# Optimization experiments

Measured on AMD Instinct MI355X. Metric: run time of the kernel, lower is better.

Reference implementation:

```python
import jax, jax.numpy as jnp
import numpy as np

B, T, D, H = 2, 2048, 768, 12
HS = D // H           # head_size = 64
FF = 4 * D            # feed_forward_multiplier = 4 -> hidden 3072
HALF = FF // 2        # SwiGLU halves hidden -> 1536
EPS = 1e-8


def rmsnorm(x, scale):
    # RMSNorm with p=-1: full-dim L2 norm / sqrt(d), then x/(rms+eps)*scale
    d = x.shape[-1]
    rms = jnp.linalg.norm(x, axis=-1, keepdims=True) * (d ** -0.5)
    return scale * (x / (rms + EPS))


def setup_inputs() -> dict:
    key = jax.random.key(0)
    ks = jax.random.split(key, 12)
    s = 0.02
    return {
        "x":  jax.random.normal(ks[0], (B, T, D), dtype=jnp.float32),
        "Wq": jax.random.normal(ks[1], (H, D, HS), dtype=jnp.float32) * s,
        "Wk": jax.random.normal(ks[2], (H, D, HS), dtype=jnp.float32) * s,
        "Wv": jax.random.normal(ks[3], (H, D, HS), dtype=jnp.float32) * s,
        "Wo": jax.random.normal(ks[4], (D, D), dtype=jnp.float32) * s,
        "bo": jnp.zeros((D,), dtype=jnp.float32),
        "W1": jax.random.normal(ks[5], (D, FF), dtype=jnp.float32) * s,
        "b1": jnp.zeros((FF,), dtype=jnp.float32),
        "W2": jax.random.normal(ks[6], (HALF, D), dtype=jnp.float32) * s,
        "b2": jnp.zeros((D,), dtype=jnp.float32),
        "g1": jnp.ones((D,), dtype=jnp.float32),
        "g2": jnp.ones((D,), dtype=jnp.float32),
    }


def reference(x, Wq, Wk, Wv, Wo, bo, W1, b1, W2, b2, g1, g2):
    Bx, Tx, Dx = x.shape
    # --- Multi-head causal attention (pre-RMSNorm, residual) ---
    h = rmsnorm(x, g1)
    q = jnp.einsum('btd,hdk->bhtk', h, Wq)
    k = jnp.einsum('btd,hdk->bhtk', h, Wk)
    v = jnp.einsum('btd,hdk->bhtk', h, Wv)
    # NOTE: original scales by C**-0.5 where C = embed_dim (not head_size)
    scores = jnp.einsum('bhtk,bhsk->bhts', q, k) * (Dx ** -0.5)
    causal = jnp.tril(jnp.ones((Tx, Tx), dtype=bool))
    scores = jnp.where(causal, scores, -jnp.inf)
    wei = jax.nn.softmax(scores, axis=-1)
    attn = jnp.einsum('bhts,bhsk->bhtk', wei, v)
    attn = attn.transpose(0, 2, 1, 3).reshape(Bx, Tx, Dx)  # concat heads
    x = x + attn @ Wo + bo
    # --- SwiGLU FFN (pre-RMSNorm, residual) ---
    h2 = rmsnorm(x, g2)
    u = h2 @ W1 + b1
    a, gate = jnp.split(u, 2, axis=-1)  # chunk: first half = value, second = gate
    x = x + (jax.nn.silu(gate) * a) @ W2 + b2
    return x
```

## Files before the change

kernel.cpp:

```cpp
#include <hip/hip_runtime.h>
#include <math.h>

#define TDIM 2048
#define DDIM 768
#define NH   12
#define NROWS 4096
#define EPSV 1e-8f
#define SCALE 0.03608439182435161f

typedef __bf16 bf16_t;
typedef bf16_t bf16x8 __attribute__((ext_vector_type(8)));
typedef bf16_t bf16x4 __attribute__((ext_vector_type(4)));
typedef float  floatx4 __attribute__((ext_vector_type(4)));

__device__ __forceinline__ void glds16(const bf16_t* g, bf16_t* l) {
    __builtin_amdgcn_global_load_lds(
        (const __attribute__((address_space(1))) void*)g,
        (__attribute__((address_space(3))) void*)l, 16, 0, 0);
}

__global__ __launch_bounds__(256) void pack_all(
    const float* __restrict__ Wq, const float* __restrict__ Wk,
    const float* __restrict__ Wv, const float* __restrict__ Wo,
    const float* __restrict__ W1, const float* __restrict__ W2,
    bf16_t* __restrict__ qkvw, bf16_t* __restrict__ wo,
    bf16_t* __restrict__ w1, bf16_t* __restrict__ w2)
{
    int bid = blockIdx.x;
    const float* src; bf16_t* dst;
    int srcld, dstld, k0, n0;
    if (bid < 144) {
        int kx = bid % 12, nx = bid / 12;
        src = Wo; dst = wo; srcld = 768; dstld = 768; k0 = kx * 64; n0 = nx * 64;
    } else if (bid < 720) {
        int t = bid - 144; int kx = t % 12, nx = t / 12;
        src = W1; dst = w1; srcld = 3072; dstld = 768; k0 = kx * 64; n0 = nx * 64;
    } else if (bid < 1008) {
        int t = bid - 720; int kx = t % 24, nx = t / 24;
        src = W2; dst = w2; srcld = 768; dstld = 1536; k0 = kx * 64; n0 = nx * 64;
    } else {
        int t = bid - 1008; int kx = t % 12, y = t / 12;
        int sel = y / 12, h = y - sel * 12;
        src = ((sel == 0) ? Wq : (sel == 1) ? Wk : Wv) + (size_t)h * 768 * 64;
        dst = qkvw + (size_t)(sel * 768 + h * 64) * 768;
        srcld = 64; dstld = 768; k0 = kx * 64; n0 = 0;
    }
    __shared__ float Ts[64][65];
    int tid = threadIdx.x;
    int r = tid >> 2, c = (tid & 3) * 16;
    const float* s = src + (size_t)(k0 + r) * srcld + n0 + c;
    #pragma unroll
    for (int i = 0; i < 4; i++) {
        float4 t = *(const float4*)(s + i * 4);
        Ts[r][c + i*4 + 0] = t.x; Ts[r][c + i*4 + 1] = t.y;
        Ts[r][c + i*4 + 2] = t.z; Ts[r][c + i*4 + 3] = t.w;
    }
    __syncthreads();
    int n = tid >> 2, kk = (tid & 3) * 16;
    bf16x8 o0, o1;
    #pragma unroll
    for (int i = 0; i < 8; i++) {
        o0[i] = (bf16_t)Ts[kk + i][n];
        o1[i] = (bf16_t)Ts[kk + 8 + i][n];
    }
    bf16_t* d = dst + (size_t)(n0 + n) * dstld + k0 + kk;
    *(bf16x8*)d = o0;
    *(bf16x8*)(d + 8) = o1;
}

__global__ __launch_bounds__(256) void rmsnorm_bf(
    const float* __restrict__ x, const float* __restrict__ g,
    bf16_t* __restrict__ out)
{
    int row = blockIdx.x;
    int tid = threadIdx.x;
    const float* xr = x + (size_t)row * DDIM;
    float v0 = xr[tid], v1 = xr[tid + 256], v2 = xr[tid + 512];
    float s = v0*v0 + v1*v1 + v2*v2;
    #pragma unroll
    for (int off = 32; off > 0; off >>= 1)
        s += __shfl_down(s, off, 64);
    __shared__ float red[4];
    __shared__ float tot;
    if ((tid & 63) == 0) red[tid >> 6] = s;
    __syncthreads();
    if (tid == 0) tot = red[0] + red[1] + red[2] + red[3];
    __syncthreads();
    float rms = sqrtf(tot * (1.0f / DDIM));
    float inv = 1.0f / (rms + EPSV);
    bf16_t* orow = out + (size_t)row * DDIM;
    orow[tid]       = (bf16_t)(g[tid]       * v0 * inv);
    orow[tid + 256] = (bf16_t)(g[tid + 256] * v1 * inv);
    orow[tid + 512] = (bf16_t)(g[tid + 512] * v2 * inv);
}

template<int TM>
__global__ __launch_bounds__(256) void gemm_bf16(
    const bf16_t* __restrict__ A, const bf16_t* __restrict__ BT, int K,
    float* __restrict__ Cf, bf16_t* __restrict__ Cb, int ldc,
    const float* __restrict__ bias, const float* __restrict__ resid)
{
    constexpr int MT = TM / 32;
    __shared__ bf16_t As0[TM][32], As1[TM][32];
    __shared__ bf16_t Bs0[128][32], Bs1[128][32];
    int tid = threadIdx.x;
    int wave = tid >> 6, lane = tid & 63;
    int lrow = lane & 15, quad = lane >> 4;
    int wm = wave >> 1, wn = wave & 1;

    int m0 = blockIdx.y * TM;
    int n0 = blockIdx.x * 128;

    int srow = lane >> 2, scol = (lane & 3) * 8;
    const bf16_t* Ag = A  + ((size_t)m0 + wave * (TM/4) + srow) * K + scol;
    const bf16_t* Bg = BT + ((size_t)n0 + wave * 32 + srow) * K + scol;

    floatx4 acc[MT][4];
    #pragma unroll
    for (int mt = 0; mt < MT; mt++)
        #pragma unroll
        for (int nt = 0; nt < 4; nt++)
            #pragma unroll
            for (int r = 0; r < 4; r++) acc[mt][nt][r] = 0.f;

    for (int k0 = 0; k0 < K; k0 += 64) {
        __syncthreads();
        #pragma unroll
        for (int i = 0; i < TM/64; i++) {
            glds16(Ag + (size_t)(i*16) * K + k0,      &As0[wave*(TM/4) + i*16][0]);
            glds16(Ag + (size_t)(i*16) * K + k0 + 32, &As1[wave*(TM/4) + i*16][0]);
        }
        #pragma unroll
        for (int i = 0; i < 2; i++) {
            glds16(Bg + (size_t)(i*16) * K + k0,      &Bs0[wave*32 + i*16][0]);
            glds16(Bg + (size_t)(i*16) * K + k0 + 32, &Bs1[wave*32 + i*16][0]);
        }
        __syncthreads();

        bf16x8 af0[MT], af1[MT], bf0[4], bf1[4];
        #pragma unroll
        for (int mt = 0; mt < MT; mt++) {
            af0[mt] = *(const bf16x8*)&As0[wm*(TM/2) + mt*16 + lrow][quad * 8];
            af1[mt] = *(const bf16x8*)&As1[wm*(TM/2) + mt*16 + lrow][quad * 8];
        }
        #pragma unroll
        for (int nt = 0; nt < 4; nt++) {
            bf0[nt] = *(const bf16x8*)&Bs0[wn*64 + nt*16 + lrow][quad * 8];
            bf1[nt] = *(const bf16x8*)&Bs1[wn*64 + nt*16 + lrow][quad * 8];
        }
        #pragma unroll
        for (int mt = 0; mt < MT; mt++)
            #pragma unroll
            for (int nt = 0; nt < 4; nt++) {
                acc[mt][nt] = __builtin_amdgcn_mfma_f32_16x16x32_bf16(
                    bf0[nt], af0[mt], acc[mt][nt], 0, 0, 0);
                acc[mt][nt] = __builtin_amdgcn_mfma_f32_16x16x32_bf16(
                    bf1[nt], af1[mt], acc[mt][nt], 0, 0, 0);
            }
    }

    int crow0 = m0 + wm * (TM/2);
    int ccol0 = n0 + wn * 64;
    #pragma unroll
    for (int mt = 0; mt < MT; mt++) {
        int row = crow0 + mt * 16 + lrow;
        #pragma unroll
        for (int nt = 0; nt < 4; nt++) {
            int col = ccol0 + nt * 16 + quad * 4;
            size_t off = (size_t)row * ldc + col;
            float4 bv = make_float4(0.f, 0.f, 0.f, 0.f);
            if (bias) bv = *(const float4*)(bias + col);
            float4 rs = make_float4(0.f, 0.f, 0.f, 0.f);
            if (resid) rs = *(const float4*)(resid + off);
            floatx4 a = acc[mt][nt];
            if (Cf) {
                float4 v;
                v.x = a[0] + bv.x + rs.x; v.y = a[1] + bv.y + rs.y;
                v.z = a[2] + bv.z + rs.z; v.w = a[3] + bv.w + rs.w;
                *(float4*)(Cf + off) = v;
            } else {
                bf16x4 v;
                v[0] = (bf16_t)(a[0] + bv.x + rs.x);
                v[1] = (bf16_t)(a[1] + bv.y + rs.y);
                v[2] = (bf16_t)(a[2] + bv.z + rs.z);
                v[3] = (bf16_t)(a[3] + bv.w + rs.w);
                *(bf16x4*)(Cb + off) = v;
            }
        }
    }
}

__global__ __launch_bounds__(256) void vt_kernel(
    const bf16_t* __restrict__ qkv, bf16_t* __restrict__ vt)
{
    __shared__ bf16_t Ts[64][72];
    int t0 = blockIdx.x * 64;
    int bh = blockIdx.y;
    int b = bh / NH, h = bh - b * NH;
    int tid = threadIdx.x;
    int r = tid >> 2, c = (tid & 3) * 16;
    const bf16_t* src = qkv + ((size_t)b * TDIM + t0 + r) * 2304 + 1536 + h * 64 + c;
    *(bf16x8*)&Ts[r][c]     = *(const bf16x8*)src;
    *(bf16x8*)&Ts[r][c + 8] = *(const bf16x8*)(src + 8);
    __syncthreads();
    int d = tid >> 2, tt = (tid & 3) * 16;
    bf16x8 o0, o1;
    #pragma unroll
    for (int i = 0; i < 8; i++) {
        o0[i] = Ts[tt + i][d];
        o1[i] = Ts[tt + 8 + i][d];
    }
    bf16_t* dst = vt + ((size_t)bh * 64 + d) * TDIM + t0 + tt;
    *(bf16x8*)dst = o0;
    *(bf16x8*)(dst + 8) = o1;
}

__global__ __launch_bounds__(256) void attn_mfma(
    const bf16_t* __restrict__ qkv, const bf16_t* __restrict__ vt,
    bf16_t* __restrict__ o)
{
    const int QS = 2304;
    int bid = blockIdx.x;
    int j = bid & 255, slot = bid >> 8;
    int qt, bh;
    if (slot == 0)      { qt = j & 31;        bh = j >> 5; }
    else if (slot == 1) { qt = 31 - (j & 31); bh = 8 + (j >> 5); }
    else                { qt = j >> 3;        bh = 16 + (j & 7); }
    int b = bh / NH, h = bh - b * NH;
    int tid = threadIdx.x;
    int wave = tid >> 6, lane = tid & 63;
    int lrow = lane & 15, quad = lane >> 4;

    __shared__ bf16_t Ks[64][72];
    __shared__ bf16_t Vt[64][72];
    __shared__ bf16_t Ps[4][16][72];

    size_t rbase = (size_t)b * TDIM;
    int q0 = qt * 64, qrow_w = q0 + wave * 16;

    const bf16_t* qp = qkv + (rbase + qrow_w + lrow) * QS + h * 64;
    bf16x8 qf[2];
    qf[0] = *(const bf16x8*)(qp + quad * 8);
    qf[1] = *(const bf16x8*)(qp + 32 + quad * 8);

    floatx4 o_acc[4];
    #pragma unroll
    for (int mt = 0; mt < 4; mt++)
        #pragma unroll
        for (int r = 0; r < 4; r++) o_acc[mt][r] = 0.f;
    float m_r = -INFINITY, l_r = 0.f;

    int srow = tid >> 2;
    int scol = (tid & 3) * 16;

    for (int s = 0; s <= qt; s++) {
        __syncthreads();
        {
            const bf16_t* kp = qkv + (rbase + s * 64 + srow) * QS + 768 + h * 64 + scol;
            *(bf16x8*)&Ks[srow][scol]     = *(const bf16x8*)kp;
            *(bf16x8*)&Ks[srow][scol + 8] = *(const bf16x8*)(kp + 8);
            const bf16_t* vp = vt + ((size_t)bh * 64 + srow) * TDIM + s * 64 + scol;
            *(bf16x8*)&Vt[srow][scol]     = *(const bf16x8*)vp;
            *(bf16x8*)&Vt[srow][scol + 8] = *(const bf16x8*)(vp + 8);
        }
        __syncthreads();

        floatx4 sfrag[4];
        #pragma unroll
        for (int nt = 0; nt < 4; nt++) {
            floatx4 a;
            #pragma unroll
            for (int r = 0; r < 4; r++) a[r] = 0.f;
            #pragma unroll
            for (int kf = 0; kf < 2; kf++) {
                bf16x8 afr = *(const bf16x8*)&Ks[nt * 16 + lrow][kf * 32 + quad * 8];
                a = __builtin_amdgcn_mfma_f32_16x16x32_bf16(afr, qf[kf], a, 0, 0, 0);
            }
            sfrag[nt] = a;
        }

        if (s == qt) {
            int qg = qrow_w + lrow;
            #pragma unroll
            for (int nt = 0; nt < 4; nt++)
                #pragma unroll
                for (int r = 0; r < 4; r++) {
                    int kc = s * 64 + nt * 16 + quad * 4 + r;
                    sfrag[nt][r] = (kc > qg) ? -INFINITY : sfrag[nt][r] * SCALE;
                }
        } else {
            #pragma unroll
            for (int nt = 0; nt < 4; nt++)
                #pragma unroll
                for (int r = 0; r < 4; r++) sfrag[nt][r] *= SCALE;
        }

        float mx = sfrag[0][0];
        #pragma unroll
        for (int nt = 0; nt < 4; nt++)
            #pragma unroll
            for (int r = 0; r < 4; r++) mx = fmaxf(mx, sfrag[nt][r]);
        mx = fmaxf(mx, __shfl_xor(mx, 16, 64));
        mx = fmaxf(mx, __shfl_xor(mx, 32, 64));
        float mn = fmaxf(m_r, mx);
        float alpha = __expf(m_r - mn);
        m_r = mn;

        float ls = 0.f;
        #pragma unroll
        for (int nt = 0; nt < 4; nt++) {
            bf16x4 pv;
            #pragma unroll
            for (int r = 0; r < 4; r++) {
                float p = __expf(sfrag[nt][r] - mn);
                ls += p;
                pv[r] = (bf16_t)p;
            }
            *(bf16x4*)&Ps[wave][lrow][nt * 16 + quad * 4] = pv;
        }
        ls += __shfl_xor(ls, 16, 64);
        ls += __shfl_xor(ls, 32, 64);
        l_r = l_r * alpha + ls;
        #pragma unroll
        for (int mt = 0; mt < 4; mt++)
            #pragma unroll
            for (int r = 0; r < 4; r++) o_acc[mt][r] *= alpha;

        #pragma unroll
        for (int kf = 0; kf < 2; kf++) {
            bf16x8 pfr = *(const bf16x8*)&Ps[wave][lrow][kf * 32 + quad * 8];
            #pragma unroll
            for (int mt = 0; mt < 4; mt++) {
                bf16x8 vfr = *(const bf16x8*)&Vt[mt * 16 + lrow][kf * 32 + quad * 8];
                o_acc[mt] = __builtin_amdgcn_mfma_f32_16x16x32_bf16(vfr, pfr, o_acc[mt], 0, 0, 0);
            }
        }
    }

    float inv = 1.0f / l_r;
    size_t rb = (rbase + qrow_w + lrow) * DDIM + h * 64;
    #pragma unroll
    for (int mt = 0; mt < 4; mt++) {
        bf16x4 ov;
        #pragma unroll
        for (int r = 0; r < 4; r++) ov[r] = (bf16_t)(o_acc[mt][r] * inv);
        *(bf16x4*)(o + rb + mt * 16 + quad * 4) = ov;
    }
}

__global__ __launch_bounds__(192) void swiglu_bf(
    const bf16_t* __restrict__ u, bf16_t* __restrict__ sw)
{
    int row = blockIdx.x;
    int j0 = threadIdx.x * 8;
    bf16x8 a = *(const bf16x8*)(u + (size_t)row * 3072 + j0);
    bf16x8 g = *(const bf16x8*)(u + (size_t)row * 3072 + 1536 + j0);
    bf16x8 r;
    #pragma unroll
    for (int i = 0; i < 8; i++) {
        float gv = (float)g[i];
        r[i] = (bf16_t)((float)a[i] * (gv / (1.0f + __expf(-gv))));
    }
    *(bf16x8*)(sw + (size_t)row * 1536 + j0) = r;
}

extern "C" void kernel_launch(void* const* d_in, const int* in_sizes, int n_in,
                              void* d_out, int out_size, void* d_ws, size_t ws_size,
                              hipStream_t stream) {
    const float* x  = (const float*)d_in[0];
    const float* Wq = (const float*)d_in[1];
    const float* Wk = (const float*)d_in[2];
    const float* Wv = (const float*)d_in[3];
    const float* Wo = (const float*)d_in[4];
    const float* bo = (const float*)d_in[5];
    const float* W1 = (const float*)d_in[6];
    const float* b1 = (const float*)d_in[7];
    const float* W2 = (const float*)d_in[8];
    const float* b2 = (const float*)d_in[9];
    const float* g1 = (const float*)d_in[10];
    const float* g2 = (const float*)d_in[11];
    float* out = (float*)d_out;
    char* ws = (char*)d_ws;

    bf16_t* qkvw_bt = (bf16_t*)(ws);
    bf16_t* wo_bt   = (bf16_t*)(ws + 3538944);
    bf16_t* w1_bt   = (bf16_t*)(ws + 4718592);
    bf16_t* w2_bt   = (bf16_t*)(ws + 9437184);
    bf16_t* h_bf    = (bf16_t*)(ws + 11796480);
    bf16_t* qkv     = (bf16_t*)(ws + 18087936);
    bf16_t* attn_bf = (bf16_t*)(ws + 36962304);
    bf16_t* u_bf    = (bf16_t*)(ws + 43253760);
    bf16_t* sw_bf   = (bf16_t*)(ws + 68419584);
    bf16_t* vt      = (bf16_t*)(ws + 81002496);

    pack_all<<<1440, 256, 0, stream>>>(Wq, Wk, Wv, Wo, W1, W2,
                                       qkvw_bt, wo_bt, w1_bt, w2_bt);

    rmsnorm_bf<<<NROWS, 256, 0, stream>>>(x, g1, h_bf);

    gemm_bf16<128><<<dim3(18, 32), 256, 0, stream>>>(
        h_bf, qkvw_bt, 768, nullptr, qkv, 2304, nullptr, nullptr);

    vt_kernel<<<dim3(32, 24), 256, 0, stream>>>(qkv, vt);

    attn_mfma<<<768, 256, 0, stream>>>(qkv, vt, attn_bf);

    gemm_bf16<64><<<dim3(6, 64), 256, 0, stream>>>(
        attn_bf, wo_bt, 768, out, nullptr, 768, bo, x);

    rmsnorm_bf<<<NROWS, 256, 0, stream>>>(out, g2, h_bf);

    gemm_bf16<128><<<dim3(24, 32), 256, 0, stream>>>(
        h_bf, w1_bt, 768, nullptr, u_bf, 3072, b1, nullptr);

    swiglu_bf<<<NROWS, 192, 0, stream>>>(u_bf, sw_bf);

    gemm_bf16<64><<<dim3(6, 64), 256, 0, stream>>>(
        sw_bf, w2_bt, 1536, out, nullptr, 768, b2, out);
}
```

Before: 266.0 us.

## Double-buffer GEMM K-loop, fuse SwiGLU into FFN1 and V-transpose into V GEMM

Rewrites the GEMM main loop to double-buffer 32-wide K slices in LDS, issuing the next slice's global-to-LDS loads before computing on the current one, with one barrier per step. Adds a V-projection GEMM that writes V directly in transposed per-head layout, which removes the separate transpose kernel and the V part of the qkv buffer. Adds an FFN1 GEMM that computes the value and gate halves together and applies SiLU gating in the epilogue, which drops the 3072-wide intermediate buffer and the SwiGLU kernel. The cost is fewer large-K tiles per step, heavier register and LDS use in the fused kernel, and scattered 8-byte stores in the V epilogue.

```diff
diff --git a/kernel.cpp b/kernel.cpp
--- a/kernel.cpp
+++ b/kernel.cpp
@@ -101,8 +101,8 @@
     const float* __restrict__ bias, const float* __restrict__ resid)
 {
     constexpr int MT = TM / 32;
-    __shared__ bf16_t As0[TM][32], As1[TM][32];
-    __shared__ bf16_t Bs0[128][32], Bs1[128][32];
+    __shared__ bf16_t As[2][TM][32];
+    __shared__ bf16_t Bs[2][128][32];
     int tid = threadIdx.x;
     int wave = tid >> 6, lane = tid & 63;
     int lrow = lane & 15, quad = lane >> 4;
@@ -115,6 +115,13 @@
     const bf16_t* Ag = A  + ((size_t)m0 + wave * (TM/4) + srow) * K + scol;
     const bf16_t* Bg = BT + ((size_t)n0 + wave * 32 + srow) * K + scol;
 
+    #pragma unroll
+    for (int i = 0; i < TM/64; i++)
+        glds16(Ag + (size_t)(i*16) * K, &As[0][wave*(TM/4) + i*16][0]);
+    #pragma unroll
+    for (int i = 0; i < 2; i++)
+        glds16(Bg + (size_t)(i*16) * K, &Bs[0][wave*32 + i*16][0]);
+
     floatx4 acc[MT][4];
     #pragma unroll
     for (int mt = 0; mt < MT; mt++)
@@ -123,40 +130,32 @@
             #pragma unroll
             for (int r = 0; r < 4; r++) acc[mt][nt][r] = 0.f;
 
-    for (int k0 = 0; k0 < K; k0 += 64) {
+    int nit = K / 32;
+    for (int it = 0; it < nit; it++) {
         __syncthreads();
-        #pragma unroll
-        for (int i = 0; i < TM/64; i++) {
-            glds16(Ag + (size_t)(i*16) * K + k0,      &As0[wave*(TM/4) + i*16][0]);
-            glds16(Ag + (size_t)(i*16) * K + k0 + 32, &As1[wave*(TM/4) + i*16][0]);
-        }
-        #pragma unroll
-        for (int i = 0; i < 2; i++) {
-            glds16(Bg + (size_t)(i*16) * K + k0,      &Bs0[wave*32 + i*16][0]);
-            glds16(Bg + (size_t)(i*16) * K + k0 + 32, &Bs1[wave*32 + i*16][0]);
-        }
-        __syncthreads();
-
-        bf16x8 af0[MT], af1[MT], bf0[4], bf1[4];
-        #pragma unroll
-        for (int mt = 0; mt < MT; mt++) {
-            af0[mt] = *(const bf16x8*)&As0[wm*(TM/2) + mt*16 + lrow][quad * 8];
-            af1[mt] = *(const bf16x8*)&As1[wm*(TM/2) + mt*16 + lrow][quad * 8];
-        }
-        #pragma unroll
-        for (int nt = 0; nt < 4; nt++) {
-            bf0[nt] = *(const bf16x8*)&Bs0[wn*64 + nt*16 + lrow][quad * 8];
-            bf1[nt] = *(const bf16x8*)&Bs1[wn*64 + nt*16 + lrow][quad * 8];
-        }
+        if (it + 1 < nit) {
+            int nb = (it + 1) & 1, ko = (it + 1) * 32;
+            #pragma unroll
+            for (int i = 0; i < TM/64; i++)
+                glds16(Ag + (size_t)(i*16) * K + ko, &As[nb][wave*(TM/4) + i*16][0]);
+            #pragma unroll
+            for (int i = 0; i < 2; i++)
+                glds16(Bg + (size_t)(i*16) * K + ko, &Bs[nb][wave*32 + i*16][0]);
+        }
+        int cb = it & 1;
+        bf16x8 af[MT], bfr[4];
         #pragma unroll
         for (int mt = 0; mt < MT; mt++)
-            #pragma unroll
-            for (int nt = 0; nt < 4; nt++) {
+            af[mt] = *(const bf16x8*)&As[cb][wm*(TM/2) + mt*16 + lrow][quad * 8];
+        #pragma unroll
+        for (int nt = 0; nt < 4; nt++)
+            bfr[nt] = *(const bf16x8*)&Bs[cb][wn*64 + nt*16 + lrow][quad * 8];
+        #pragma unroll
+        for (int mt = 0; mt < MT; mt++)
+            #pragma unroll
+            for (int nt = 0; nt < 4; nt++)
                 acc[mt][nt] = __builtin_amdgcn_mfma_f32_16x16x32_bf16(
-                    bf0[nt], af0[mt], acc[mt][nt], 0, 0, 0);
-                acc[mt][nt] = __builtin_amdgcn_mfma_f32_16x16x32_bf16(
-                    bf1[nt], af1[mt], acc[mt][nt], 0, 0, 0);
-            }
+                    bfr[nt], af[mt], acc[mt][nt], 0, 0, 0);
     }
 
     int crow0 = m0 + wm * (TM/2);
@@ -190,36 +189,177 @@
     }
 }
 
-__global__ __launch_bounds__(256) void vt_kernel(
-    const bf16_t* __restrict__ qkv, bf16_t* __restrict__ vt)
+__global__ __launch_bounds__(256) void gemm_v(
+    const bf16_t* __restrict__ A, const bf16_t* __restrict__ BT,
+    bf16_t* __restrict__ vt)
 {
-    __shared__ bf16_t Ts[64][72];
-    int t0 = blockIdx.x * 64;
-    int bh = blockIdx.y;
-    int b = bh / NH, h = bh - b * NH;
+    const int K = 768;
+    __shared__ bf16_t As[2][128][32];
+    __shared__ bf16_t Bs[2][128][32];
     int tid = threadIdx.x;
-    int r = tid >> 2, c = (tid & 3) * 16;
-    const bf16_t* src = qkv + ((size_t)b * TDIM + t0 + r) * 2304 + 1536 + h * 64 + c;
-    *(bf16x8*)&Ts[r][c]     = *(const bf16x8*)src;
-    *(bf16x8*)&Ts[r][c + 8] = *(const bf16x8*)(src + 8);
-    __syncthreads();
-    int d = tid >> 2, tt = (tid & 3) * 16;
-    bf16x8 o0, o1;
-    #pragma unroll
-    for (int i = 0; i < 8; i++) {
-        o0[i] = Ts[tt + i][d];
-        o1[i] = Ts[tt + 8 + i][d];
-    }
-    bf16_t* dst = vt + ((size_t)bh * 64 + d) * TDIM + t0 + tt;
-    *(bf16x8*)dst = o0;
-    *(bf16x8*)(dst + 8) = o1;
+    int wave = tid >> 6, lane = tid & 63;
+    int lrow = lane & 15, quad = lane >> 4;
+    int wm = wave >> 1, wn = wave & 1;
+
+    int m0 = blockIdx.y * 128;
+    int n0 = blockIdx.x * 128;
+
+    int srow = lane >> 2, scol = (lane & 3) * 8;
+    const bf16_t* Ag = A  + ((size_t)m0 + wave * 32 + srow) * K + scol;
+    const bf16_t* Bg = BT + ((size_t)n0 + wave * 32 + srow) * K + scol;
+
+    #pragma unroll
+    for (int i = 0; i < 2; i++) {
+        glds16(Ag + (size_t)(i*16) * K, &As[0][wave*32 + i*16][0]);
+        glds16(Bg + (size_t)(i*16) * K, &Bs[0][wave*32 + i*16][0]);
+    }
+
+    floatx4 acc[4][4];
+    #pragma unroll
+    for (int mt = 0; mt < 4; mt++)
+        #pragma unroll
+        for (int nt = 0; nt < 4; nt++)
+            #pragma unroll
+            for (int r = 0; r < 4; r++) acc[mt][nt][r] = 0.f;
+
+    int nit = K / 32;
+    for (int it = 0; it < nit; it++) {
+        __syncthreads();
+        if (it + 1 < nit) {
+            int nb = (it + 1) & 1, ko = (it + 1) * 32;
+            #pragma unroll
+            for (int i = 0; i < 2; i++) {
+                glds16(Ag + (size_t)(i*16) * K + ko, &As[nb][wave*32 + i*16][0]);
+                glds16(Bg + (size_t)(i*16) * K + ko, &Bs[nb][wave*32 + i*16][0]);
+            }
+        }
+        int cb = it & 1;
+        bf16x8 af[4], bfr[4];
+        #pragma unroll
+        for (int mt = 0; mt < 4; mt++)
+            af[mt] = *(const bf16x8*)&As[cb][wm*64 + mt*16 + lrow][quad * 8];
+        #pragma unroll
+        for (int nt = 0; nt < 4; nt++)
+            bfr[nt] = *(const bf16x8*)&Bs[cb][wn*64 + nt*16 + lrow][quad * 8];
+        #pragma unroll
+        for (int mt = 0; mt < 4; mt++)
+            #pragma unroll
+            for (int nt = 0; nt < 4; nt++)
+                acc[mt][nt] = __builtin_amdgcn_mfma_f32_16x16x32_bf16(
+                    af[mt], bfr[nt], acc[mt][nt], 0, 0, 0);
+    }
+
+    #pragma unroll
+    for (int nt = 0; nt < 4; nt++) {
+        int d = n0 + wn * 64 + nt * 16 + lrow;
+        int h = d >> 6, dl = d & 63;
+        #pragma unroll
+        for (int mt = 0; mt < 4; mt++) {
+            int mg = m0 + wm * 64 + mt * 16 + quad * 4;
+            int b = mg >> 11, tl = mg & 2047;
+            bf16x4 v;
+            #pragma unroll
+            for (int r = 0; r < 4; r++) v[r] = (bf16_t)acc[mt][nt][r];
+            *(bf16x4*)(vt + (((size_t)(b * NH + h) * 64 + dl) * TDIM + tl)) = v;
+        }
+    }
+}
+
+__global__ __launch_bounds__(256) void gemm_ffn1(
+    const bf16_t* __restrict__ A, const bf16_t* __restrict__ W1t,
+    const float* __restrict__ b1, bf16_t* __restrict__ sw)
+{
+    const int K = 768;
+    __shared__ bf16_t As[2][64][32];
+    __shared__ bf16_t Ba[2][128][32];
+    __shared__ bf16_t Bg[2][128][32];
+    int tid = threadIdx.x;
+    int wave = tid >> 6, lane = tid & 63;
+    int lrow = lane & 15, quad = lane >> 4;
+    int wm = wave >> 1, wn = wave & 1;
+
+    int m0 = blockIdx.y * 64;
+    int n0 = blockIdx.x * 128;
+
+    int srow = lane >> 2, scol = (lane & 3) * 8;
+    const bf16_t* Agp = A   + ((size_t)m0 + wave * 16 + srow) * K + scol;
+    const bf16_t* Bap = W1t + ((size_t)n0 + wave * 32 + srow) * K + scol;
+    const bf16_t* Bgp = W1t + ((size_t)(1536 + n0) + wave * 32 + srow) * K + scol;
+
+    glds16(Agp, &As[0][wave*16][0]);
+    #pragma unroll
+    for (int i = 0; i < 2; i++) {
+        glds16(Bap + (size_t)(i*16) * K, &Ba[0][wave*32 + i*16][0]);
+        glds16(Bgp + (size_t)(i*16) * K, &Bg[0][wave*32 + i*16][0]);
+    }
+
+    floatx4 acc_a[2][4], acc_g[2][4];
+    #pragma unroll
+    for (int mt = 0; mt < 2; mt++)
+        #pragma unroll
+        for (int nt = 0; nt < 4; nt++)
+            #pragma unroll
+            for (int r = 0; r < 4; r++) { acc_a[mt][nt][r] = 0.f; acc_g[mt][nt][r] = 0.f; }
+
+    int nit = K / 32;
+    for (int it = 0; it < nit; it++) {
+        __syncthreads();
+        if (it + 1 < nit) {
+            int nb = (it + 1) & 1, ko = (it + 1) * 32;
+            glds16(Agp + ko, &As[nb][wave*16][0]);
+            #pragma unroll
+            for (int i = 0; i < 2; i++) {
+                glds16(Bap + (size_t)(i*16) * K + ko, &Ba[nb][wave*32 + i*16][0]);
+                glds16(Bgp + (size_t)(i*16) * K + ko, &Bg[nb][wave*32 + i*16][0]);
+            }
+        }
+        int cb = it & 1;
+        bf16x8 af[2], ba[4], bg[4];
+        #pragma unroll
+        for (int mt = 0; mt < 2; mt++)
+            af[mt] = *(const bf16x8*)&As[cb][wm*32 + mt*16 + lrow][quad * 8];
+        #pragma unroll
+        for (int nt = 0; nt < 4; nt++) {
+            ba[nt] = *(const bf16x8*)&Ba[cb][wn*64 + nt*16 + lrow][quad * 8];
+            bg[nt] = *(const bf16x8*)&Bg[cb][wn*64 + nt*16 + lrow][quad * 8];
+        }
+        #pragma unroll
+        for (int mt = 0; mt < 2; mt++)
+            #pragma unroll
+            for (int nt = 0; nt < 4; nt++) {
+                acc_a[mt][nt] = __builtin_amdgcn_mfma_f32_16x16x32_bf16(
+                    ba[nt], af[mt], acc_a[mt][nt], 0, 0, 0);
+                acc_g[mt][nt] = __builtin_amdgcn_mfma_f32_16x16x32_bf16(
+                    bg[nt], af[mt], acc_g[mt][nt], 0, 0, 0);
+            }
+    }
+
+    #pragma unroll
+    for (int mt = 0; mt < 2; mt++) {
+        int row = m0 + wm * 32 + mt * 16 + lrow;
+        #pragma unroll
+        for (int nt = 0; nt < 4; nt++) {
+            int col = n0 + wn * 64 + nt * 16 + quad * 4;
+            float4 bva = *(const float4*)(b1 + col);
+            float4 bvg = *(const float4*)(b1 + 1536 + col);
+            float av[4] = { acc_a[mt][nt][0] + bva.x, acc_a[mt][nt][1] + bva.y,
+                            acc_a[mt][nt][2] + bva.z, acc_a[mt][nt][3] + bva.w };
+            float gv[4] = { acc_g[mt][nt][0] + bvg.x, acc_g[mt][nt][1] + bvg.y,
+                            acc_g[mt][nt][2] + bvg.z, acc_g[mt][nt][3] + bvg.w };
+            bf16x4 v;
+            #pragma unroll
+            for (int r = 0; r < 4; r++)
+                v[r] = (bf16_t)(av[r] * (gv[r] / (1.0f + __expf(-gv[r]))));
+            *(bf16x4*)(sw + (size_t)row * 1536 + col) = v;
+        }
+    }
 }
 
 __global__ __launch_bounds__(256) void attn_mfma(
-    const bf16_t* __restrict__ qkv, const bf16_t* __restrict__ vt,
+    const bf16_t* __restrict__ qk, const bf16_t* __restrict__ vt,
     bf16_t* __restrict__ o)
 {
-    const int QS = 2304;
+    const int QS = 1536;
     int bid = blockIdx.x;
     int j = bid & 255, slot = bid >> 8;
     int qt, bh;
@@ -238,7 +378,7 @@
     size_t rbase = (size_t)b * TDIM;
     int q0 = qt * 64, qrow_w = q0 + wave * 16;
 
-    const bf16_t* qp = qkv + (rbase + qrow_w + lrow) * QS + h * 64;
+    const bf16_t* qp = qk + (rbase + qrow_w + lrow) * QS + h * 64;
     bf16x8 qf[2];
     qf[0] = *(const bf16x8*)(qp + quad * 8);
     qf[1] = *(const bf16x8*)(qp + 32 + quad * 8);
@@ -256,7 +396,7 @@
     for (int s = 0; s <= qt; s++) {
         __syncthreads();
         {
-            const bf16_t* kp = qkv + (rbase + s * 64 + srow) * QS + 768 + h * 64 + scol;
+            const bf16_t* kp = qk + (rbase + s * 64 + srow) * QS + 768 + h * 64 + scol;
             *(bf16x8*)&Ks[srow][scol]     = *(const bf16x8*)kp;
             *(bf16x8*)&Ks[srow][scol + 8] = *(const bf16x8*)(kp + 8);
             const bf16_t* vp = vt + ((size_t)bh * 64 + srow) * TDIM + s * 64 + scol;
@@ -346,22 +486,6 @@
         for (int r = 0; r < 4; r++) ov[r] = (bf16_t)(o_acc[mt][r] * inv);
         *(bf16x4*)(o + rb + mt * 16 + quad * 4) = ov;
     }
-}
-
-__global__ __launch_bounds__(192) void swiglu_bf(
-    const bf16_t* __restrict__ u, bf16_t* __restrict__ sw)
-{
-    int row = blockIdx.x;
-    int j0 = threadIdx.x * 8;
-    bf16x8 a = *(const bf16x8*)(u + (size_t)row * 3072 + j0);
-    bf16x8 g = *(const bf16x8*)(u + (size_t)row * 3072 + 1536 + j0);
-    bf16x8 r;
-    #pragma unroll
-    for (int i = 0; i < 8; i++) {
-        float gv = (float)g[i];
-        r[i] = (bf16_t)((float)a[i] * (gv / (1.0f + __expf(-gv))));
-    }
-    *(bf16x8*)(sw + (size_t)row * 1536 + j0) = r;
 }
 
 extern "C" void kernel_launch(void* const* d_in, const int* in_sizes, int n_in,
@@ -387,33 +511,29 @@
     bf16_t* w1_bt   = (bf16_t*)(ws + 4718592);
     bf16_t* w2_bt   = (bf16_t*)(ws + 9437184);
     bf16_t* h_bf    = (bf16_t*)(ws + 11796480);
-    bf16_t* qkv     = (bf16_t*)(ws + 18087936);
-    bf16_t* attn_bf = (bf16_t*)(ws + 36962304);
-    bf16_t* u_bf    = (bf16_t*)(ws + 43253760);
-    bf16_t* sw_bf   = (bf16_t*)(ws + 68419584);
-    bf16_t* vt      = (bf16_t*)(ws + 81002496);
+    bf16_t* qk      = (bf16_t*)(ws + 18087936);
+    bf16_t* attn_bf = (bf16_t*)(ws + 30670848);
+    bf16_t* sw_bf   = (bf16_t*)(ws + 36962304);
+    bf16_t* vt      = (bf16_t*)(ws + 49545216);
 
     pack_all<<<1440, 256, 0, stream>>>(Wq, Wk, Wv, Wo, W1, W2,
                                        qkvw_bt, wo_bt, w1_bt, w2_bt);
 
     rmsnorm_bf<<<NROWS, 256, 0, stream>>>(x, g1, h_bf);
 
-    gemm_bf16<128><<<dim3(18, 32), 256, 0, stream>>>(
-        h_bf, qkvw_bt, 768, nullptr, qkv, 2304, nullptr, nullptr);
-
-    vt_kernel<<<dim3(32, 24), 256, 0, stream>>>(qkv, vt);
-
-    attn_mfma<<<768, 256, 0, stream>>>(qkv, vt, attn_bf);
+    gemm_bf16<128><<<dim3(12, 32), 256, 0, stream>>>(
+        h_bf, qkvw_bt, 768, nullptr, qk, 1536, nullptr, nullptr);
+
+    gemm_v<<<dim3(6, 32), 256, 0, stream>>>(h_bf, qkvw_bt + (size_t)1536 * 768, vt);
+
+    attn_mfma<<<768, 256, 0, stream>>>(qk, vt, attn_bf);
 
     gemm_bf16<64><<<dim3(6, 64), 256, 0, stream>>>(
         attn_bf, wo_bt, 768, out, nullptr, 768, bo, x);
 
     rmsnorm_bf<<<NROWS, 256, 0, stream>>>(out, g2, h_bf);
 
-    gemm_bf16<128><<<dim3(24, 32), 256, 0, stream>>>(
-        h_bf, w1_bt, 768, nullptr, u_bf, 3072, b1, nullptr);
-
-    swiglu_bf<<<NROWS, 192, 0, stream>>>(u_bf, sw_bf);
+    gemm_ffn1<<<dim3(12, 64), 256, 0, stream>>>(h_bf, w1_bt, b1, sw_bf);
 
     gemm_bf16<64><<<dim3(6, 64), 256, 0, stream>>>(
         sw_bf, w2_bt, 1536, out, nullptr, 768, b2, out);
```

Result: slower. 287.6 us (+8.1%).
